# Performance work log

Measured on AMD Instinct MI355X. Metric: run time of the kernel, lower is better.

## Reference

```python
import jax, jax.numpy as jnp
import numpy as np

DEPTH = 12
NODE_SIZE = 64
IN_SCALE = 1.0
SCALE = 0.1
IN_W = 1.8
SIZE = 2 ** DEPTH - 1          # 4095 total nodes
REST = SIZE - 1                # 4094 non-root nodes
M_BATCH = 128


def setup_inputs() -> dict:
    key = jax.random.key(0)
    k1, k2, k3 = jax.random.split(key, 3)
    weights = IN_W + 1e-4 * jax.random.normal(k1, (SIZE,), dtype=jnp.float32)
    noise_root = jax.random.normal(k2, (M_BATCH, NODE_SIZE, 1), dtype=jnp.float32)
    noise_rest = jax.random.normal(k3, (M_BATCH, NODE_SIZE, REST), dtype=jnp.float32)
    return {"weights": weights, "noise_root": noise_root, "noise_rest": noise_rest, "M": M_BATCH}


def reference(weights, noise_root, noise_rest, M):
    # Root: Normal(0, in_scale).rsample((M, node_size, 1))
    root = IN_SCALE * noise_root                      # (M, node, 1)
    samples_levels = [root]
    m_levels = []
    scale_levels = []
    off = 0
    for d in range(1, DEPTH):
        n = 2 ** d
        w = jax.nn.sigmoid(weights[off:off + n])       # (n,)
        parent = jnp.arange(n) // 2                    # half-index parent lookup
        m = w[None, None, :] * samples_levels[-1][:, :, parent]   # (M, node, n)
        sc = jnp.broadcast_to(((1.0 - w) * SCALE)[None, None, :], m.shape)
        samp = m + sc * noise_rest[:, :, off:off + n]  # reparameterized rsample
        samples_levels.append(samp)
        m_levels.append(m)
        scale_levels.append(sc)
        off += n
    samples = jnp.concatenate(samples_levels[::-1], axis=2)  # (M, node, 4095)
    ms = jnp.concatenate(m_levels[::-1], axis=2)              # (M, node, 4094)
    scales = jnp.concatenate(scale_levels[::-1], axis=2)      # (M, node, 4094)
    return samples, ms, scales
```

## Files before the change

### kernel.cpp

```cpp
#include <hip/hip_runtime.h>


constexpr int   kDepth = 12;
constexpr int   kSize  = 4095;
constexpr int   kRest  = 4094;
constexpr int   kRows  = 8192;
constexpr float kScale = 0.1f;
constexpr int   kBlock = 256;

__device__ __align__(16) float g_wcol[4096];
__device__ __align__(16) float g_sccol[4096];

__global__ __launch_bounds__(kBlock) void lgt_precompute(
    const float* __restrict__ weights)
{
    int t = blockIdx.x * kBlock + threadIdx.x;
    if (t < kRest) {
        int d = 31 - __clz(t + 2);
        int c = t + 4098 - 3 * (1 << d);
        float w = 1.0f / (1.0f + __expf(-weights[t]));
        g_wcol[c]  = w;
        g_sccol[c] = (1.0f - w) * kScale;
    }
}

__global__ __launch_bounds__(kBlock) void lgt_main(
    const float* __restrict__ noise_root,
    const float* __restrict__ noise_rest,
    float* __restrict__ samples,
    float* __restrict__ ms,
    float* __restrict__ scales)
{
    __shared__ float s[4096];

    const int row = blockIdx.x;
    const int tid = threadIdx.x;
    const float* __restrict__ nr = noise_rest + (size_t)row * kRest;

    if (tid == 0) s[4094] = noise_root[row];
    __syncthreads();

    if (tid < 2) {
        int c = 4092 + tid;
        s[c] = fmaf(g_sccol[c], nr[tid], g_wcol[c] * s[4094]);
    }
    __syncthreads();

    int off = 2;
    for (int d = 2; d < kDepth; ++d) {
        const int n = 1 << d;
        const int colbase = 4096 - (n << 1);
        for (int i0 = tid << 2; i0 < n; i0 += (kBlock << 2)) {
            const int c = colbase + i0;
            const float4 w4  = *(const float4*)(g_wcol  + c);
            const float4 sc4 = *(const float4*)(g_sccol + c);
            const float2 nz0 = *(const float2*)(nr + off + i0);
            const float2 nz1 = *(const float2*)(nr + off + i0 + 2);
            const int p = (c >> 1) + 2048;
            const float p0 = s[p], p1 = s[p + 1];
            float4 v;
            v.x = fmaf(sc4.x, nz0.x, w4.x * p0);
            v.y = fmaf(sc4.y, nz0.y, w4.y * p0);
            v.z = fmaf(sc4.z, nz1.x, w4.z * p1);
            v.w = fmaf(sc4.w, nz1.y, w4.w * p1);
            *(float4*)(s + c) = v;
        }
        __syncthreads();
        off += n;
    }

    {
        const size_t rb = (size_t)row * (size_t)kSize;
        float* __restrict__ sr = samples + rb;
        const int h = (int)((4u - ((unsigned)rb & 3u)) & 3u);
        if (tid < h) sr[tid] = s[tid];
        const int nch = (kSize - h) >> 2;
        for (int k = tid; k < nch; k += kBlock) {
            const int c = h + (k << 2);
            float4 v;
            v.x = s[c]; v.y = s[c + 1]; v.z = s[c + 2]; v.w = s[c + 3];
            *(float4*)(sr + c) = v;
        }
        const int done = h + (nch << 2);
        if (tid >= 8 && tid < 8 + (kSize - done)) {
            const int c = done + tid - 8;
            sr[c] = s[c];
        }
    }
    {
        const size_t rb = (size_t)row * (size_t)kRest;
        float* __restrict__ mr = ms + rb;
        float* __restrict__ cr = scales + rb;
        const int h = (int)((4u - ((unsigned)rb & 3u)) & 3u);
        if (tid < h) {
            const int c = tid;
            mr[c] = g_wcol[c] * s[(c >> 1) + 2048];
            cr[c] = g_sccol[c];
        }
        const int nch = (kRest - h) >> 2;
        for (int k = tid; k < nch; k += kBlock) {
            const int c = h + (k << 2);
            const float2 wa = *(const float2*)(g_wcol  + c);
            const float2 wb = *(const float2*)(g_wcol  + c + 2);
            const float2 ca = *(const float2*)(g_sccol + c);
            const float2 cb = *(const float2*)(g_sccol + c + 2);
            const int p = (c >> 1) + 2048;
            const float p0 = s[p], p1 = s[p + 1];
            float4 mv, cv;
            mv.x = wa.x * p0; mv.y = wa.y * p0;
            mv.z = wb.x * p1; mv.w = wb.y * p1;
            cv.x = ca.x; cv.y = ca.y; cv.z = cb.x; cv.w = cb.y;
            *(float4*)(mr + c) = mv;
            *(float4*)(cr + c) = cv;
        }
        const int done = h + (nch << 2);
        if (tid >= 8 && tid < 8 + (kRest - done)) {
            const int c = done + tid - 8;
            mr[c] = g_wcol[c] * s[(c >> 1) + 2048];
            cr[c] = g_sccol[c];
        }
    }
}

extern "C" void kernel_launch(void* const* d_in, const int* in_sizes, int n_in,
                              void* d_out, int out_size, void* d_ws, size_t ws_size,
                              hipStream_t stream)
{
    const float* weights    = (const float*)d_in[0];
    const float* noise_root = (const float*)d_in[1];
    const float* noise_rest = (const float*)d_in[2];

    float* out     = (float*)d_out;
    float* samples = out;
    float* ms      = samples + (size_t)kRows * kSize;
    float* scales  = ms      + (size_t)kRows * kRest;

    lgt_precompute<<<(kRest + kBlock - 1) / kBlock, kBlock, 0, stream>>>(weights);
    lgt_main<<<kRows, kBlock, 0, stream>>>(noise_root, noise_rest,
                                           samples, ms, scales);
}
```

Measured before the change: 144.1 us.

## Process four rows per 1024-thread block for aligned contiguous output stores

Each block now handles four consecutive rows with 1024 threads, keeping all four rows' samples in shared memory. The tree levels are spread across rows, so the small top levels keep more threads busy. Because four rows of 4095 and 4094 floats are multiples of 4, whole-block output regions are 16-byte aligned, which removes the per-row head and tail scalar stores. The cost is 64KB of shared memory per block, which lowers occupancy, a branchy path for float4 chunks that cross a row boundary in ms/scales, and scalar shared stores in the tree loop.

```diff
diff --git a/kernel.cpp b/kernel.cpp
--- a/kernel.cpp
+++ b/kernel.cpp
@@ -1,21 +1,23 @@
 #include <hip/hip_runtime.h>
 
 
-constexpr int   kDepth = 12;
-constexpr int   kSize  = 4095;
-constexpr int   kRest  = 4094;
-constexpr int   kRows  = 8192;
-constexpr float kScale = 0.1f;
-constexpr int   kBlock = 256;
+constexpr int   kDepth  = 12;
+constexpr int   kRows   = 8192;
+constexpr float kScale  = 0.1f;
+constexpr int   kBlkPre = 256;
+constexpr int   kBlk    = 1024;
+constexpr int   kG      = 4;
+constexpr int   kSampB  = kG * 4095;
+constexpr int   kRestB  = kG * 4094;
 
 __device__ __align__(16) float g_wcol[4096];
 __device__ __align__(16) float g_sccol[4096];
 
-__global__ __launch_bounds__(kBlock) void lgt_precompute(
+__global__ __launch_bounds__(kBlkPre) void lgt_precompute(
     const float* __restrict__ weights)
 {
-    int t = blockIdx.x * kBlock + threadIdx.x;
-    if (t < kRest) {
+    int t = blockIdx.x * kBlkPre + threadIdx.x;
+    if (t < 4094) {
         int d = 31 - __clz(t + 2);
         int c = t + 4098 - 3 * (1 << d);
         float w = 1.0f / (1.0f + __expf(-weights[t]));
@@ -24,100 +26,103 @@
     }
 }
 
-__global__ __launch_bounds__(kBlock) void lgt_main(
+__global__ __launch_bounds__(kBlk) void lgt_main(
     const float* __restrict__ noise_root,
     const float* __restrict__ noise_rest,
     float* __restrict__ samples,
     float* __restrict__ ms,
     float* __restrict__ scales)
 {
-    __shared__ float s[4096];
+    __shared__ float s[kSampB];
 
-    const int row = blockIdx.x;
-    const int tid = threadIdx.x;
-    const float* __restrict__ nr = noise_rest + (size_t)row * kRest;
+    const int blk  = blockIdx.x;
+    const int tid  = threadIdx.x;
+    const int row0 = blk << 2;
 
-    if (tid == 0) s[4094] = noise_root[row];
+    if (tid < 4) {
+        s[tid * 4095 + 4094] = noise_root[row0 + tid];
+    }
     __syncthreads();
 
-    if (tid < 2) {
-        int c = 4092 + tid;
-        s[c] = fmaf(g_sccol[c], nr[tid], g_wcol[c] * s[4094]);
+    if (tid < 8) {
+        const int r = tid >> 1, i = tid & 1;
+        const int c = 4092 + i;
+        const float par = s[r * 4095 + 4094];
+        s[r * 4095 + c] =
+            fmaf(g_sccol[c], noise_rest[(size_t)(row0 + r) * 4094 + i],
+                 g_wcol[c] * par);
     }
     __syncthreads();
 
     int off = 2;
     for (int d = 2; d < kDepth; ++d) {
-        const int n = 1 << d;
+        const int n       = 1 << d;
         const int colbase = 4096 - (n << 1);
-        for (int i0 = tid << 2; i0 < n; i0 += (kBlock << 2)) {
-            const int c = colbase + i0;
+        const int qshift  = d - 2;
+        const int qmask   = (n >> 2) - 1;
+        for (int t = tid; t < n; t += kBlk) {
+            const int r  = t >> qshift;
+            const int i0 = (t & qmask) << 2;
+            const int c  = colbase + i0;
+            const int lb = r * 4095;
             const float4 w4  = *(const float4*)(g_wcol  + c);
             const float4 sc4 = *(const float4*)(g_sccol + c);
-            const float2 nz0 = *(const float2*)(nr + off + i0);
-            const float2 nz1 = *(const float2*)(nr + off + i0 + 2);
-            const int p = (c >> 1) + 2048;
+            const float* nrp = noise_rest + (size_t)(row0 + r) * 4094 + off + i0;
+            const float2 nz0 = *(const float2*)(nrp);
+            const float2 nz1 = *(const float2*)(nrp + 2);
+            const int p = lb + (c >> 1) + 2048;
             const float p0 = s[p], p1 = s[p + 1];
-            float4 v;
-            v.x = fmaf(sc4.x, nz0.x, w4.x * p0);
-            v.y = fmaf(sc4.y, nz0.y, w4.y * p0);
-            v.z = fmaf(sc4.z, nz1.x, w4.z * p1);
-            v.w = fmaf(sc4.w, nz1.y, w4.w * p1);
-            *(float4*)(s + c) = v;
+            s[lb + c]     = fmaf(sc4.x, nz0.x, w4.x * p0);
+            s[lb + c + 1] = fmaf(sc4.y, nz0.y, w4.y * p0);
+            s[lb + c + 2] = fmaf(sc4.z, nz1.x, w4.z * p1);
+            s[lb + c + 3] = fmaf(sc4.w, nz1.y, w4.w * p1);
         }
         __syncthreads();
         off += n;
     }
 
     {
-        const size_t rb = (size_t)row * (size_t)kSize;
-        float* __restrict__ sr = samples + rb;
-        const int h = (int)((4u - ((unsigned)rb & 3u)) & 3u);
-        if (tid < h) sr[tid] = s[tid];
-        const int nch = (kSize - h) >> 2;
-        for (int k = tid; k < nch; k += kBlock) {
-            const int c = h + (k << 2);
-            float4 v;
-            v.x = s[c]; v.y = s[c + 1]; v.z = s[c + 2]; v.w = s[c + 3];
-            *(float4*)(sr + c) = v;
-        }
-        const int done = h + (nch << 2);
-        if (tid >= 8 && tid < 8 + (kSize - done)) {
-            const int c = done + tid - 8;
-            sr[c] = s[c];
+        float* __restrict__ sb = samples + (size_t)blk * kSampB;
+        for (int k = tid; k < (kSampB >> 2); k += kBlk) {
+            const int j = k << 2;
+            const float4 v = *(const float4*)(s + j);
+            *(float4*)(sb + j) = v;
         }
     }
+
     {
-        const size_t rb = (size_t)row * (size_t)kRest;
-        float* __restrict__ mr = ms + rb;
-        float* __restrict__ cr = scales + rb;
-        const int h = (int)((4u - ((unsigned)rb & 3u)) & 3u);
-        if (tid < h) {
-            const int c = tid;
-            mr[c] = g_wcol[c] * s[(c >> 1) + 2048];
-            cr[c] = g_sccol[c];
-        }
-        const int nch = (kRest - h) >> 2;
-        for (int k = tid; k < nch; k += kBlock) {
-            const int c = h + (k << 2);
-            const float2 wa = *(const float2*)(g_wcol  + c);
-            const float2 wb = *(const float2*)(g_wcol  + c + 2);
-            const float2 ca = *(const float2*)(g_sccol + c);
-            const float2 cb = *(const float2*)(g_sccol + c + 2);
-            const int p = (c >> 1) + 2048;
-            const float p0 = s[p], p1 = s[p + 1];
+        float* __restrict__ mb = ms     + (size_t)blk * kRestB;
+        float* __restrict__ cb = scales + (size_t)blk * kRestB;
+        for (int k = tid; k < (kRestB >> 2); k += kBlk) {
+            const int j  = k << 2;
+            const int r0 = (j >= 4094) + (j >= 8188) + (j >= 12282);
+            const int r3 = ((j + 3) >= 4094) + ((j + 3) >= 8188) + ((j + 3) >= 12282);
             float4 mv, cv;
-            mv.x = wa.x * p0; mv.y = wa.y * p0;
-            mv.z = wb.x * p1; mv.w = wb.y * p1;
-            cv.x = ca.x; cv.y = ca.y; cv.z = cb.x; cv.w = cb.y;
-            *(float4*)(mr + c) = mv;
-            *(float4*)(cr + c) = cv;
-        }
-        const int done = h + (nch << 2);
-        if (tid >= 8 && tid < 8 + (kRest - done)) {
-            const int c = done + tid - 8;
-            mr[c] = g_wcol[c] * s[(c >> 1) + 2048];
-            cr[c] = g_sccol[c];
+            if (r0 == r3) {
+                const int c = j - r0 * 4094;
+                const float2 wa = *(const float2*)(g_wcol  + c);
+                const float2 wb = *(const float2*)(g_wcol  + c + 2);
+                const float2 ca = *(const float2*)(g_sccol + c);
+                const float2 cb2= *(const float2*)(g_sccol + c + 2);
+                const int p = r0 * 4095 + (c >> 1) + 2048;
+                const float p0 = s[p], p1 = s[p + 1];
+                mv.x = wa.x * p0; mv.y = wa.y * p0;
+                mv.z = wb.x * p1; mv.w = wb.y * p1;
+                cv.x = ca.x; cv.y = ca.y; cv.z = cb2.x; cv.w = cb2.y;
+            } else {
+                float* mvp = (float*)&mv;
+                float* cvp = (float*)&cv;
+                #pragma unroll
+                for (int e = 0; e < 4; ++e) {
+                    const int je = j + e;
+                    const int r  = (je >= 4094) + (je >= 8188) + (je >= 12282);
+                    const int c  = je - r * 4094;
+                    mvp[e] = g_wcol[c] * s[r * 4095 + (c >> 1) + 2048];
+                    cvp[e] = g_sccol[c];
+                }
+            }
+            *(float4*)(mb + j) = mv;
+            *(float4*)(cb + j) = cv;
         }
     }
 }
@@ -132,10 +137,10 @@
 
     float* out     = (float*)d_out;
     float* samples = out;
-    float* ms      = samples + (size_t)kRows * kSize;
-    float* scales  = ms      + (size_t)kRows * kRest;
+    float* ms      = samples + (size_t)kRows * 4095;
+    float* scales  = ms      + (size_t)kRows * 4094;
 
-    lgt_precompute<<<(kRest + kBlock - 1) / kBlock, kBlock, 0, stream>>>(weights);
-    lgt_main<<<kRows, kBlock, 0, stream>>>(noise_root, noise_rest,
-                                           samples, ms, scales);
+    lgt_precompute<<<(4094 + kBlkPre - 1) / kBlkPre, kBlkPre, 0, stream>>>(weights);
+    lgt_main<<<kRows / kG, kBlk, 0, stream>>>(noise_root, noise_rest,
+                                              samples, ms, scales);
 }
```

Result: slower. 152.3 us (+5.7%).
